# Kernel optimization log

Measured on AMD Instinct MI355X. Metric: run time of the kernel, lower is better.

## Reference

```python
import jax, jax.numpy as jnp
import numpy as np

EPS = 1e-8
LN_EPS = 1e-5
NEG = -1e9
H, E, D, P = 4, 32, 8, 64          # heads, embed_dim, head_dim, particles (= input_dim)
N_LAYERS, N_CLS = 4, 2
N_BATCH = 2048
F_EXTRA = 60                        # x feature channels; F_EXTRA + 4 == P == input_dim


def _ln(x):
    m = jnp.mean(x, -1, keepdims=True)
    v = jnp.mean((x - m) ** 2, -1, keepdims=True)
    return (x - m) * jax.lax.rsqrt(v + LN_EPS)


def _lin(x, w, b):
    return x @ w.T + b


def _gelu(x):
    return jax.nn.gelu(x, approximate=False)


def _mha(q_in, kv, in_w, in_b, out_w, out_b, attn_bias, kpm):
    # torch nn.MultiheadAttention, batch_first=False. q_in: (L,N,E), kv: (S,N,E)
    L, N, _ = q_in.shape
    S = kv.shape[0]
    q = _lin(q_in, in_w[:E], in_b[:E]) * (D ** -0.5)
    k = _lin(kv, in_w[E:2 * E], in_b[E:2 * E])
    v = _lin(kv, in_w[2 * E:], in_b[2 * E:])
    q = q.reshape(L, N, H, D); k = k.reshape(S, N, H, D); v = v.reshape(S, N, H, D)
    s = jnp.einsum('lnhd,snhd->nhls', q, k)
    if attn_bias is not None:
        s = s + attn_bias.reshape(N, H, L, S)
    s = jnp.where(kpm[:, None, None, :], NEG, s)
    a = jax.nn.softmax(s, -1)
    o = jnp.einsum('nhls,snhd->lnhd', a, v).reshape(L, N, E)
    return _lin(o, out_w, out_b)


def _jet_features(v):
    # vectorized calculate_jet_features_; v: (N,4,P). All pair features are symmetric,
    # diagonal stays zero (python loop skipped i==j), features are detached.
    e, px, py, pz = v[:, 0], v[:, 1], v[:, 2], v[:, 3]
    pt = jnp.sqrt(px ** 2 + py ** 2 + EPS)
    y = 0.5 * jnp.log((e + pz + EPS) / (e - pz + EPS))
    phi = jnp.mod(jnp.arctan2(py, px + EPS), 2.0 * np.pi)   # already in [0, 2pi)
    r = lambda a: a[:, :, None]
    c = lambda a: a[:, None, :]
    dist = (r(px) + c(px)) ** 2 + (r(py) + c(py)) ** 2 + (r(pz) + c(pz)) ** 2
    delta = jnp.sqrt(jnp.abs((r(y) - c(y)) ** 2 + (r(phi) - c(phi)) ** 2))
    pmin = jnp.minimum(r(pt), c(pt))
    kt = pmin * delta
    z = pmin / (r(pt) + c(pt) + EPS)
    m2 = r(e) ** 2 + c(e) ** 2 - dist
    f = jnp.stack([delta, kt, z, m2], axis=1)               # (N,4,P,P)
    f = f * (1.0 - jnp.eye(v.shape[2], dtype=f.dtype))
    return jax.lax.stop_gradient(f)


def _conv2d(x, w, b, stride, pad):
    y = jax.lax.conv_general_dilated(x, w, (stride, stride), [(pad, pad), (pad, pad)],
                                     dimension_numbers=('NCHW', 'OIHW', 'NCHW'))
    return y + b[None, :, None, None]


def _forward(x, four_momenta, jet_inputs, bn_w, bn_b, e1_w, e1_b, e2_w, e2_b,
             c1_w, c1_b, c2_w, c2_b,
             pb_in_w, pb_in_b, pb_out_w, pb_out_b, pb_f1_w, pb_f1_b, pb_f2_w, pb_f2_b, pb_wres,
             cb_in_w, cb_in_b, cb_out_w, cb_out_b, cb_f1_w, cb_f1_b, cb_f2_w, cb_f2_b, cb_wres,
             cb_cattn, cls_token, norm_w, norm_b, m1_w, m1_b, mh_w, mh_b, mf_w, mf_b):
    N = x.shape[0]
    xc = jnp.concatenate([x, four_momenta], axis=1)                 # (N, P, P): channels == particles
    kpm = ~(jnp.arange(P)[None, :] < jet_inputs[:, 1][:, None])     # (N, P) True = padded key
    xb = jnp.transpose(xc, (0, 2, 1))                               # (N, C=P, L=input_dim)
    mu = jnp.mean(xb, axis=(0, 2), keepdims=True)
    var = jnp.var(xb, axis=(0, 2), keepdims=True)
    xb = (xb - mu) * jax.lax.rsqrt(var + LN_EPS) * bn_w[None, :, None] + bn_b[None, :, None]
    h = jnp.transpose(xb, (2, 0, 1))                                # (seq, N, P)
    h = _gelu(_lin(_ln(h), e1_w, e1_b))
    h = _gelu(_lin(_ln(h), e2_w, e2_b))                             # (P, N, E)
    # --- PairEmbed: pairwise kinematic features -> 2 convs -> per-head attention bias
    f = _jet_features(four_momenta)                                 # (N, 4, P, P)
    cpe = _conv2d(f, c1_w, c1_b, 4, 0)                              # (N, H, 16, 16)
    cpe = _conv2d(cpe, c2_w, c2_b, 2, 1)                            # (N, H, 9, 9)
    bias = cpe.reshape(N * H, 9, 9)
    bias = jnp.pad(bias, ((0, 0), (0, P - 9), (0, P - 9)))          # additive bias zero-padded to (N*H,P,P)
    # --- particle blocks
    for i in range(N_LAYERS):
        res = h
        a = _ln(h)
        a = _mha(a, a, pb_in_w[i], pb_in_b[i], pb_out_w[i], pb_out_b[i], bias, kpm)
        h = _ln(a) + res
        res = h
        g = _gelu(_lin(_ln(h), pb_f1_w[i], pb_f1_b[i]))
        g = _lin(_ln(g), pb_f2_w[i], pb_f2_b[i])
        h = g + pb_wres[i] * res
    # --- class-attention blocks
    kpm_cls = jnp.concatenate([jnp.zeros((N, 1), dtype=bool), kpm], axis=1)
    cls = jnp.broadcast_to(cls_token, (1, N, E))
    for i in range(N_CLS):
        res = cls
        u = _ln(jnp.concatenate([cls, h], axis=0))                  # pre_attn_norm on keys/values only
        a = _mha(cls, u, cb_in_w[i], cb_in_b[i], cb_out_w[i], cb_out_b[i], None, kpm_cls)
        # tbhd,h->tbdh then reshape flattens as (d, h) order, matching torch
        a = jnp.einsum('tbhd,h->tbdh', a.reshape(1, N, H, D), cb_cattn[i]).reshape(1, N, E)
        cls = _ln(a) + res
        res = cls
        g = _gelu(_lin(_ln(cls), cb_f1_w[i], cb_f1_b[i]))
        g = _lin(_ln(g), cb_f2_w[i], cb_f2_b[i])
        cls = g + cb_wres[i] * res
    # --- head: affine LayerNorm + MLP (the two transposes in MLP cancel)
    z = (_ln(cls) * norm_w + norm_b)[0]                             # (N, E)
    z = jax.nn.relu(_lin(z, m1_w, m1_b))
    z = jax.nn.relu(_lin(z, mh_w, mh_b))
    z = jax.nn.sigmoid(_lin(z, mf_w, mf_b))                         # (N, 1)
    return z.reshape(-1)


def setup_inputs():
    key = jax.random.key(0)
    ks = jax.random.split(key, 40)
    w = lambda k, s: (0.05 * jax.random.normal(k, s)).astype(jnp.float32)
    p3 = jax.random.normal(ks[0], (N_BATCH, 3, P), dtype=jnp.float32)
    en = jnp.sqrt(jnp.sum(p3 ** 2, axis=1, keepdims=True) + 0.1)    # physical: E > |pz|
    four_momenta = jnp.concatenate([en, p3], axis=1)
    return {
        'x': jax.random.normal(ks[1], (N_BATCH, F_EXTRA, P), dtype=jnp.float32),
        'four_momenta': four_momenta,
        'jet_inputs': jax.random.randint(ks[2], (N_BATCH, 2), 1, P + 1),
        'bn_w': jnp.ones((P,), jnp.float32), 'bn_b': jnp.zeros((P,), jnp.float32),
        'e1_w': w(ks[3], (64, P)), 'e1_b': w(ks[4], (64,)),
        'e2_w': w(ks[5], (E, 64)), 'e2_b': w(ks[6], (E,)),
        'c1_w': w(ks[7], (H, 4, 4, 4)), 'c1_b': w(ks[8], (H,)),
        'c2_w': w(ks[9], (H, H, 2, 2)), 'c2_b': w(ks[10], (H,)),
        'pb_in_w': w(ks[11], (N_LAYERS, 3 * E, E)), 'pb_in_b': w(ks[12], (N_LAYERS, 3 * E)),
        'pb_out_w': w(ks[13], (N_LAYERS, E, E)), 'pb_out_b': w(ks[14], (N_LAYERS, E)),
        'pb_f1_w': w(ks[15], (N_LAYERS, 2 * E, E)), 'pb_f1_b': w(ks[16], (N_LAYERS, 2 * E)),
        'pb_f2_w': w(ks[17], (N_LAYERS, E, 2 * E)), 'pb_f2_b': w(ks[18], (N_LAYERS, E)),
        'pb_wres': jnp.ones((N_LAYERS, E), jnp.float32),
        'cb_in_w': w(ks[19], (N_CLS, 3 * E, E)), 'cb_in_b': w(ks[20], (N_CLS, 3 * E)),
        'cb_out_w': w(ks[21], (N_CLS, E, E)), 'cb_out_b': w(ks[22], (N_CLS, E)),
        'cb_f1_w': w(ks[23], (N_CLS, 2 * E, E)), 'cb_f1_b': w(ks[24], (N_CLS, 2 * E)),
        'cb_f2_w': w(ks[25], (N_CLS, E, 2 * E)), 'cb_f2_b': w(ks[26], (N_CLS, E)),
        'cb_wres': jnp.ones((N_CLS, E), jnp.float32),
        'cb_cattn': jnp.ones((N_CLS, H), jnp.float32),
        'cls_token': w(ks[27], (1, 1, E)),
        'norm_w': jnp.ones((E,), jnp.float32), 'norm_b': jnp.zeros((E,), jnp.float32),
        'm1_w': w(ks[28], (32, E)), 'm1_b': w(ks[29], (32,)),
        'mh_w': w(ks[30], (32, 32)), 'mh_b': w(ks[31], (32,)),
        'mf_w': w(ks[32], (1, 32)), 'mf_b': w(ks[33], (1,)),
    }


def reference(x, four_momenta, jet_inputs, bn_w, bn_b, e1_w, e1_b, e2_w, e2_b,
              c1_w, c1_b, c2_w, c2_b,
              pb_in_w, pb_in_b, pb_out_w, pb_out_b, pb_f1_w, pb_f1_b, pb_f2_w, pb_f2_b, pb_wres,
              cb_in_w, cb_in_b, cb_out_w, cb_out_b, cb_f1_w, cb_f1_b, cb_f2_w, cb_f2_b, cb_wres,
              cb_cattn, cls_token, norm_w, norm_b, m1_w, m1_b, mh_w, mh_b, mf_w, mf_b):
    return _forward(x, four_momenta, jet_inputs, bn_w, bn_b, e1_w, e1_b, e2_w, e2_b,
                    c1_w, c1_b, c2_w, c2_b,
                    pb_in_w, pb_in_b, pb_out_w, pb_out_b, pb_f1_w, pb_f1_b, pb_f2_w, pb_f2_b, pb_wres,
                    cb_in_w, cb_in_b, cb_out_w, cb_out_b, cb_f1_w, cb_f1_b, cb_f2_w, cb_f2_b, cb_wres,
                    cb_cattn, cls_token, norm_w, norm_b, m1_w, m1_b, mh_w, mh_b, mf_w, mf_b)
```

## Files before the change

### kernel.cpp

```cpp
#include <hip/hip_runtime.h>


__device__ __forceinline__ float4 ld4(const float* p){ return *reinterpret_cast<const float4*>(p); }
__device__ __forceinline__ void st4(float* p, float4 v){ *reinterpret_cast<float4*>(p) = v; }
__device__ __forceinline__ float dot4(float4 a, float4 b){ return a.x*b.x + a.y*b.y + a.z*b.z + a.w*b.w; }
__device__ __forceinline__ float geluf(float v){ return 0.5f*v*(1.0f + erff(v*0.70710678118654752f)); }

__global__ void bn_stats_partial(const float* __restrict__ x, const float* __restrict__ fm,
                                 float* __restrict__ part) {
  int p  = threadIdx.x & 63;
  int rg = threadIdx.x >> 6;
  float s = 0.f, s2 = 0.f;
  for (int R = blockIdx.x*4 + rg; R < 2048*64; R += 1024) {
    int n_ = R >> 6, c = R & 63;
    float v = (c < 60) ? x[n_*3840 + c*64 + p] : fm[n_*256 + (c-60)*64 + p];
    s += v; s2 += v*v;
  }
  __shared__ float sm[256], sm2[256];
  sm[threadIdx.x] = s; sm2[threadIdx.x] = s2;
  __syncthreads();
  if (threadIdx.x < 64) {
    part[blockIdx.x*128 + p]      = sm[p]+sm[64+p]+sm[128+p]+sm[192+p];
    part[blockIdx.x*128 + 64 + p] = sm2[p]+sm2[64+p]+sm2[128+p]+sm2[192+p];
  }
}

__global__ void bn_stats_final(const float* __restrict__ part, float* __restrict__ stats) {
  int p = threadIdx.x;
  float s = 0.f, s2 = 0.f;
  for (int b = 0; b < 256; b++){ s += part[b*128+p]; s2 += part[b*128+64+p]; }
  float mean = s * (1.f/131072.f);
  float var  = s2 * (1.f/131072.f) - mean*mean;
  stats[p]      = mean;
  stats[64+p]   = rsqrtf(var + 1e-5f);
}

__device__ __forceinline__ void ln_rows32(const float* src, float* dst, int tid){
  int r = tid>>2, g = tid&3;
  const float* row = src + r*36 + g*8;
  float4 a = ld4(row), b = ld4(row+4);
  float s = a.x+a.y+a.z+a.w + b.x+b.y+b.z+b.w;
  s += __shfl_xor(s,1); s += __shfl_xor(s,2);
  float mean = s * 0.03125f;
  float4 da = make_float4(a.x-mean,a.y-mean,a.z-mean,a.w-mean);
  float4 db = make_float4(b.x-mean,b.y-mean,b.z-mean,b.w-mean);
  float q = dot4(da,da) + dot4(db,db);
  q += __shfl_xor(q,1); q += __shfl_xor(q,2);
  float irs = rsqrtf(q*0.03125f + 1e-5f);
  float* drow = dst + r*36 + g*8;
  st4(drow,   make_float4(da.x*irs, da.y*irs, da.z*irs, da.w*irs));
  st4(drow+4, make_float4(db.x*irs, db.y*irs, db.z*irs, db.w*irs));
}

__device__ __forceinline__ void ln_rows64(const float* src, float* dst, int tid){
  int r = tid>>2, g = tid&3;
  const float* row = src + r*68 + g*16;
  float4 v0 = ld4(row), v1 = ld4(row+4), v2 = ld4(row+8), v3 = ld4(row+12);
  float s = v0.x+v0.y+v0.z+v0.w + v1.x+v1.y+v1.z+v1.w
          + v2.x+v2.y+v2.z+v2.w + v3.x+v3.y+v3.z+v3.w;
  s += __shfl_xor(s,1); s += __shfl_xor(s,2);
  float mean = s * 0.015625f;
  float4 d0 = make_float4(v0.x-mean,v0.y-mean,v0.z-mean,v0.w-mean);
  float4 d1 = make_float4(v1.x-mean,v1.y-mean,v1.z-mean,v1.w-mean);
  float4 d2 = make_float4(v2.x-mean,v2.y-mean,v2.z-mean,v2.w-mean);
  float4 d3 = make_float4(v3.x-mean,v3.y-mean,v3.z-mean,v3.w-mean);
  float q = dot4(d0,d0)+dot4(d1,d1)+dot4(d2,d2)+dot4(d3,d3);
  q += __shfl_xor(q,1); q += __shfl_xor(q,2);
  float irs = rsqrtf(q*0.015625f + 1e-5f);
  float* drow = dst + r*68 + g*16;
  st4(drow,    make_float4(d0.x*irs,d0.y*irs,d0.z*irs,d0.w*irs));
  st4(drow+4,  make_float4(d1.x*irs,d1.y*irs,d1.z*irs,d1.w*irs));
  st4(drow+8,  make_float4(d2.x*irs,d2.y*irs,d2.z*irs,d2.w*irs));
  st4(drow+12, make_float4(d3.x*irs,d3.y*irs,d3.z*irs,d3.w*irs));
}

__global__ __launch_bounds__(256) void k_feat(
    const float* __restrict__ fm,
    const float* __restrict__ c1w_g, const float* __restrict__ c1b_g,
    const float* __restrict__ c2w_g, const float* __restrict__ c2b_g,
    float* __restrict__ G_bias)
{
  const int n   = blockIdx.x;
  const int tid = threadIdx.x;
  __shared__ float PQ[448];
  __shared__ float C1O[1024];
  __shared__ float CW[328];

  if (tid < 64) {
    int p = tid;
    float e_  = fm[n*256 + p];
    float px_ = fm[n*256 + 64 + p];
    float py_ = fm[n*256 + 128 + p];
    float pz_ = fm[n*256 + 192 + p];
    float pt_ = sqrtf(px_*px_ + py_*py_ + 1e-8f);
    float y_  = 0.5f * logf((e_ + pz_ + 1e-8f) / (e_ - pz_ + 1e-8f));
    float ph_ = atan2f(py_, px_ + 1e-8f);
    if (ph_ < 0.f) ph_ += 6.283185307179586f;
    PQ[0*64+p]=e_; PQ[1*64+p]=px_; PQ[2*64+p]=py_; PQ[3*64+p]=pz_;
    PQ[4*64+p]=pt_; PQ[5*64+p]=y_; PQ[6*64+p]=ph_;
  }
  CW[tid < 256 ? tid : 0] = c1w_g[tid < 256 ? tid : 0];
  if (tid < 4)  CW[256+tid] = c1b_g[tid];
  if (tid < 64) CW[260+tid] = c2w_g[tid];
  if (tid < 4)  CW[324+tid] = c2b_g[tid];
  __syncthreads();

  {
    int ho = tid>>4, wo = tid&15;
    float a0=0.f,a1=0.f,a2=0.f,a3=0.f;
    #pragma unroll 1
    for (int kh=0; kh<4; kh++){
      int r = ho*4+kh;
      float er=PQ[r], pxr=PQ[64+r], pyr=PQ[128+r], pzr=PQ[192+r], ptr_=PQ[256+r], yr=PQ[320+r], phr=PQ[384+r];
      #pragma unroll
      for (int kw=0; kw<4; kw++){
        int c = wo*4+kw;
        if (r == c) continue;
        float ec=PQ[c], pxc=PQ[64+c], pyc=PQ[128+c], pzc=PQ[192+c], ptc=PQ[256+c], yc=PQ[320+c], phc=PQ[384+c];
        float dy = yr-yc, dp = phr-phc;
        float delta = sqrtf(fabsf(dy*dy + dp*dp));
        float pmin = fminf(ptr_, ptc);
        float kt = pmin * delta;
        float zz = pmin / (ptr_ + ptc + 1e-8f);
        float sx_ = pxr+pxc, sy_ = pyr+pyc, sz_ = pzr+pzc;
        float m2 = er*er + ec*ec - (sx_*sx_ + sy_*sy_ + sz_*sz_);
        int wb = kh*4+kw;
        a0 += delta*CW[0*64+wb] + kt*CW[0*64+16+wb] + zz*CW[0*64+32+wb] + m2*CW[0*64+48+wb];
        a1 += delta*CW[1*64+wb] + kt*CW[1*64+16+wb] + zz*CW[1*64+32+wb] + m2*CW[1*64+48+wb];
        a2 += delta*CW[2*64+wb] + kt*CW[2*64+16+wb] + zz*CW[2*64+32+wb] + m2*CW[2*64+48+wb];
        a3 += delta*CW[3*64+wb] + kt*CW[3*64+16+wb] + zz*CW[3*64+32+wb] + m2*CW[3*64+48+wb];
      }
    }
    C1O[0*256 + tid] = a0 + CW[256+0];
    C1O[1*256 + tid] = a1 + CW[256+1];
    C1O[2*256 + tid] = a2 + CW[256+2];
    C1O[3*256 + tid] = a3 + CW[256+3];
  }
  __syncthreads();

  for (int idx = tid; idx < 324; idx += 256) {
    int co = idx/81, rem = idx%81, i = rem/9, j = rem%9;
    float s = CW[324+co];
    #pragma unroll
    for (int ci=0; ci<4; ci++){
      #pragma unroll
      for (int kh=0; kh<2; kh++){
        int ri = 2*i - 1 + kh;
        if (ri < 0 || ri >= 16) continue;
        #pragma unroll
        for (int kw=0; kw<2; kw++){
          int cj = 2*j - 1 + kw;
          if (cj < 0 || cj >= 16) continue;
          s += CW[260 + co*16 + ci*4 + kh*2 + kw] * C1O[ci*256 + ri*16 + cj];
        }
      }
    }
    G_bias[n*324 + idx] = s;
  }
}

__global__ __launch_bounds__(256, 3) void k_embed2(
    const float* __restrict__ x, const float* __restrict__ fm,
    const float* __restrict__ stats,
    const float* __restrict__ bn_w, const float* __restrict__ bn_b,
    const float* __restrict__ e1w, const float* __restrict__ e1b,
    const float* __restrict__ e2w, const float* __restrict__ e2b,
    float* __restrict__ G_h)
{
  const int n   = blockIdx.x;
  const int tid = threadIdx.x;

  __shared__ __align__(16) float SX[64*68];
  __shared__ __align__(16) float SY[64*68];
  __shared__ __align__(16) float SW[4448];
  __shared__ float SSTAT[128];

  if (tid < 64) {
    float mu = stats[tid], rs = stats[64+tid];
    float sc = rs * bn_w[tid];
    SSTAT[tid]      = sc;
    SSTAT[64+tid]   = bn_b[tid] - mu*sc;
  }
  __syncthreads();

  {
    int p = tid & 63;
    float sc = SSTAT[p], sh = SSTAT[64+p];
    for (int c = tid>>6; c < 64; c += 4) {
      float v = (c < 60) ? x[n*3840 + c*64 + p] : fm[n*256 + (c-60)*64 + p];
      SX[c*68 + p] = v*sc + sh;
    }
  }
  __syncthreads();

  ln_rows64(SX, SY, tid);
  for (int idx = tid; idx < 4096; idx += 256){ SW[(idx>>6)*68 + (idx&63)] = e1w[idx]; }
  for (int idx = tid; idx < 64; idx += 256) SW[4352+idx] = e1b[idx];
  __syncthreads();

  {
    int tg = tid>>4, og = tid&15;
    float acc[4][4];
    #pragma unroll
    for (int o=0;o<4;o++){ float b = SW[4352+o*16+og];
      #pragma unroll
      for (int i=0;i<4;i++) acc[i][o] = b; }
    #pragma unroll 2
    for (int j=0;j<64;j+=4){
      float4 av[4], wv[4];
      #pragma unroll
      for (int i=0;i<4;i++) av[i] = ld4(SY + (tg*4+i)*68 + j);
      #pragma unroll
      for (int o=0;o<4;o++) wv[o] = ld4(SW + (o*16+og)*68 + j);
      #pragma unroll
      for (int i=0;i<4;i++)
        #pragma unroll
        for (int o=0;o<4;o++) acc[i][o] += dot4(av[i], wv[o]);
    }
    __syncthreads();
    #pragma unroll
    for (int i=0;i<4;i++)
      #pragma unroll
      for (int o=0;o<4;o++) SX[(tg*4+i)*68 + o*16+og] = geluf(acc[i][o]);
  }
  __syncthreads();

  ln_rows64(SX, SY, tid);
  for (int idx = tid; idx < 2048; idx += 256){ SW[(idx>>6)*68 + (idx&63)] = e2w[idx]; }
  for (int idx = tid; idx < 32; idx += 256) SW[4352+idx] = e2b[idx];
  __syncthreads();

  {
    int tg = tid>>4, og = tid&15;
    float acc[4][2];
    #pragma unroll
    for (int o=0;o<2;o++){ float b = SW[4352+o*16+og];
      #pragma unroll
      for (int i=0;i<4;i++) acc[i][o] = b; }
    #pragma unroll 2
    for (int j=0;j<64;j+=4){
      float4 av[4], wv[2];
      #pragma unroll
      for (int i=0;i<4;i++) av[i] = ld4(SY + (tg*4+i)*68 + j);
      #pragma unroll
      for (int o=0;o<2;o++) wv[o] = ld4(SW + (o*16+og)*68 + j);
      #pragma unroll
      for (int i=0;i<4;i++)
        #pragma unroll
        for (int o=0;o<2;o++) acc[i][o] += dot4(av[i], wv[o]);
    }
    #pragma unroll
    for (int i=0;i<4;i++)
      #pragma unroll
      for (int o=0;o<2;o++) G_h[n*2048 + (tg*4+i)*32 + o*16+og] = geluf(acc[i][o]);
  }
}

__global__ __launch_bounds__(256, 3) void k_layer(
    const int* __restrict__ ji,
    const float* __restrict__ in_w,  const float* __restrict__ in_b,
    const float* __restrict__ out_w, const float* __restrict__ out_b,
    const float* __restrict__ f1w,   const float* __restrict__ f1b,
    const float* __restrict__ f2w,   const float* __restrict__ f2b,
    const float* __restrict__ wres,
    float* __restrict__ G_h, const float* __restrict__ G_bias)
{
  const int n   = blockIdx.x;
  const int tid = threadIdx.x;

  __shared__ __align__(16) float SH[64*36];
  __shared__ __align__(16) float SX[64*36];
  __shared__ __align__(16) float SY[64*68];
  __shared__ __align__(16) float SW[3584];
  __shared__ float SBIAS[324];
  __shared__ int s_njet;

  if (tid == 0) s_njet = ji[n*2+1];
  for (int idx = tid; idx < 512; idx += 256) {
    float4 v = ld4(G_h + n*2048 + idx*4);
    int t = idx>>3, e = (idx&7)*4;
    st4(&SH[t*36 + e], v);
  }
  for (int idx = tid; idx < 324; idx += 256) SBIAS[idx] = G_bias[n*324 + idx];
  __syncthreads();

  ln_rows32(SH, SX, tid);
  for (int idx = tid; idx < 3072; idx += 256){ SW[(idx>>5)*36 + (idx&31)] = in_w[idx]; }
  for (int idx = tid; idx < 96; idx += 256) SW[3456+idx] = in_b[idx];
  __syncthreads();

  {
    int tg = tid>>4, og = tid&15;
    float acc[4][4];
    #pragma unroll
    for (int o=0;o<4;o++){ float b = SW[3456+32+o*16+og];
      #pragma unroll
      for (int i=0;i<4;i++) acc[i][o] = b; }
    #pragma unroll 2
    for (int j=0;j<32;j+=4){
      float4 av[4], wv[4];
      #pragma unroll
      for (int i=0;i<4;i++) av[i] = ld4(SX + (tg*4+i)*36 + j);
      #pragma unroll
      for (int o=0;o<4;o++) wv[o] = ld4(SW + (32+o*16+og)*36 + j);
      #pragma unroll
      for (int i=0;i<4;i++)
        #pragma unroll
        for (int o=0;o<4;o++) acc[i][o] += dot4(av[i], wv[o]);
    }
    #pragma unroll
    for (int i=0;i<4;i++)
      #pragma unroll
      for (int o=0;o<4;o++){
        int ew = 32 + o*16+og, t = tg*4+i;
        if (ew < 64) SY[(ew-32)*68 + t] = acc[i][o];
        else         SY[2176 + (ew-64)*68 + t] = acc[i][o];
      }
  }
  __syncthreads();

  float od[8];
  {
    int hh = tid>>6, l = tid&63;
    float qd[8];
    #pragma unroll
    for (int d=0;d<8;d++){
      int e = hh*8+d;
      float a_ = SW[3456+e];
      #pragma unroll
      for (int k=0;k<8;k++) a_ += dot4(ld4(SX + l*36 + k*4), ld4(SW + e*36 + k*4));
      qd[d] = a_ * 0.35355339059327373f;
    }
    int njet = s_njet;
    float m = -3.4e38f, lsum = 0.f;
    #pragma unroll
    for (int d=0;d<8;d++) od[d] = 0.f;
    #pragma unroll 1
    for (int s0 = 0; s0 < 64; s0 += 16) {
      float sc[16];
      #pragma unroll
      for (int j=0;j<16;j++) sc[j]=0.f;
      #pragma unroll
      for (int d=0;d<8;d++){
        const float* kr = SY + (hh*8+d)*68 + s0;
        float qv = qd[d];
        #pragma unroll
        for (int j=0;j<16;j+=4){
          float4 kv4 = ld4(kr+j);
          sc[j]  +=qv*kv4.x; sc[j+1]+=qv*kv4.y;
          sc[j+2]+=qv*kv4.z; sc[j+3]+=qv*kv4.w;
        }
      }
      float cm = -3.4e38f;
      #pragma unroll
      for (int j=0;j<16;j++){
        int s = s0+j;
        float a_ = sc[j];
        if (s0 == 0 && l < 9 && j < 9) a_ += SBIAS[hh*81 + l*9 + j];
        a_ = (s >= njet) ? -1000000000.0f : a_;
        sc[j] = a_;
        cm = fmaxf(cm, a_);
      }
      float nm = fmaxf(m, cm);
      float corr = __expf(m - nm);
      lsum *= corr;
      #pragma unroll
      for (int d=0;d<8;d++) od[d] *= corr;
      #pragma unroll
      for (int j=0;j<16;j++){ sc[j] = __expf(sc[j]-nm); lsum += sc[j]; }
      #pragma unroll
      for (int d=0;d<8;d++){
        const float* vr = SY + 2176 + (hh*8+d)*68 + s0;
        float a_ = 0.f;
        #pragma unroll
        for (int j=0;j<16;j+=4){
          float4 vv = ld4(vr+j);
          a_ += sc[j]*vv.x + sc[j+1]*vv.y + sc[j+2]*vv.z + sc[j+3]*vv.w;
        }
        od[d] += a_;
      }
      m = nm;
    }
    float inv = 1.f/lsum;
    #pragma unroll
    for (int d=0;d<8;d++) od[d] *= inv;
  }
  __syncthreads();
  {
    int hh = tid>>6, l = tid&63;
    st4(&SX[l*36 + hh*8],     make_float4(od[0],od[1],od[2],od[3]));
    st4(&SX[l*36 + hh*8 + 4], make_float4(od[4],od[5],od[6],od[7]));
  }
  for (int idx = tid; idx < 1024; idx += 256){ SW[(idx>>5)*36 + (idx&31)] = out_w[idx]; }
  for (int idx = tid; idx < 32; idx += 256) SW[3456+idx] = out_b[idx];
  __syncthreads();

  {
    int tg = tid>>4, og = tid&15;
    float acc[4][2];
    #pragma unroll
    for (int o=0;o<2;o++){ float b = SW[3456+o*16+og];
      #pragma unroll
      for (int i=0;i<4;i++) acc[i][o] = b; }
    #pragma unroll 2
    for (int j=0;j<32;j+=4){
      float4 av[4], wv[2];
      #pragma unroll
      for (int i=0;i<4;i++) av[i] = ld4(SX + (tg*4+i)*36 + j);
      #pragma unroll
      for (int o=0;o<2;o++) wv[o] = ld4(SW + (o*16+og)*36 + j);
      #pragma unroll
      for (int i=0;i<4;i++)
        #pragma unroll
        for (int o=0;o<2;o++) acc[i][o] += dot4(av[i], wv[o]);
    }
    #pragma unroll
    for (int i=0;i<4;i++)
      #pragma unroll
      for (int o=0;o<2;o++) SY[(tg*4+i)*36 + o*16+og] = acc[i][o];
  }
  __syncthreads();

  {
    int r = tid>>2, g = tid&3;
    const float* row = SY + r*36 + g*8;
    float4 a = ld4(row), b = ld4(row+4);
    float s = a.x+a.y+a.z+a.w + b.x+b.y+b.z+b.w;
    s += __shfl_xor(s,1); s += __shfl_xor(s,2);
    float mean = s * 0.03125f;
    float4 da = make_float4(a.x-mean,a.y-mean,a.z-mean,a.w-mean);
    float4 db = make_float4(b.x-mean,b.y-mean,b.z-mean,b.w-mean);
    float q = dot4(da,da) + dot4(db,db);
    q += __shfl_xor(q,1); q += __shfl_xor(q,2);
    float irs = rsqrtf(q*0.03125f + 1e-5f);
    float* hrow = SH + r*36 + g*8;
    float4 ha = ld4(hrow), hb = ld4(hrow+4);
    st4(hrow,   make_float4(da.x*irs+ha.x, da.y*irs+ha.y, da.z*irs+ha.z, da.w*irs+ha.w));
    st4(hrow+4, make_float4(db.x*irs+hb.x, db.y*irs+hb.y, db.z*irs+hb.z, db.w*irs+hb.w));
  }
  __syncthreads();

  ln_rows32(SH, SX, tid);
  for (int idx = tid; idx < 2048; idx += 256){ SW[(idx>>5)*36 + (idx&31)] = f1w[idx]; }
  for (int idx = tid; idx < 64; idx += 256) SW[3456+idx] = f1b[idx];
  __syncthreads();

  {
    int tg = tid>>4, og = tid&15;
    float acc[4][4];
    #pragma unroll
    for (int o=0;o<4;o++){ float b = SW[3456+o*16+og];
      #pragma unroll
      for (int i=0;i<4;i++) acc[i][o] = b; }
    #pragma unroll 2
    for (int j=0;j<32;j+=4){
      float4 av[4], wv[4];
      #pragma unroll
      for (int i=0;i<4;i++) av[i] = ld4(SX + (tg*4+i)*36 + j);
      #pragma unroll
      for (int o=0;o<4;o++) wv[o] = ld4(SW + (o*16+og)*36 + j);
      #pragma unroll
      for (int i=0;i<4;i++)
        #pragma unroll
        for (int o=0;o<4;o++) acc[i][o] += dot4(av[i], wv[o]);
    }
    #pragma unroll
    for (int i=0;i<4;i++)
      #pragma unroll
      for (int o=0;o<4;o++) SY[(tg*4+i)*68 + o*16+og] = geluf(acc[i][o]);
  }
  __syncthreads();

  {
    int r = tid>>2, g = tid&3;
    float* row = SY + r*68 + g*16;
    float4 v0 = ld4(row), v1 = ld4(row+4), v2 = ld4(row+8), v3 = ld4(row+12);
    float s = v0.x+v0.y+v0.z+v0.w + v1.x+v1.y+v1.z+v1.w
            + v2.x+v2.y+v2.z+v2.w + v3.x+v3.y+v3.z+v3.w;
    s += __shfl_xor(s,1); s += __shfl_xor(s,2);
    float mean = s * 0.015625f;
    float4 d0 = make_float4(v0.x-mean,v0.y-mean,v0.z-mean,v0.w-mean);
    float4 d1 = make_float4(v1.x-mean,v1.y-mean,v1.z-mean,v1.w-mean);
    float4 d2 = make_float4(v2.x-mean,v2.y-mean,v2.z-mean,v2.w-mean);
    float4 d3 = make_float4(v3.x-mean,v3.y-mean,v3.z-mean,v3.w-mean);
    float q = dot4(d0,d0)+dot4(d1,d1)+dot4(d2,d2)+dot4(d3,d3);
    q += __shfl_xor(q,1); q += __shfl_xor(q,2);
    float irs = rsqrtf(q*0.015625f + 1e-5f);
    st4(row,    make_float4(d0.x*irs,d0.y*irs,d0.z*irs,d0.w*irs));
    st4(row+4,  make_float4(d1.x*irs,d1.y*irs,d1.z*irs,d1.w*irs));
    st4(row+8,  make_float4(d2.x*irs,d2.y*irs,d2.z*irs,d2.w*irs));
    st4(row+12, make_float4(d3.x*irs,d3.y*irs,d3.z*irs,d3.w*irs));
  }
  for (int idx = tid; idx < 2048; idx += 256){ SW[(idx>>6)*68 + (idx&63)] = f2w[idx]; }
  for (int idx = tid; idx < 32; idx += 256){ SW[3456+idx] = f2b[idx]; SW[3488+idx] = wres[idx]; }
  __syncthreads();

  {
    int tg = tid>>4, og = tid&15;
    float acc[4][2];
    #pragma unroll
    for (int o=0;o<2;o++){ float b = SW[3456+o*16+og];
      #pragma unroll
      for (int i=0;i<4;i++) acc[i][o] = b; }
    #pragma unroll 2
    for (int j=0;j<64;j+=4){
      float4 av[4], wv[2];
      #pragma unroll
      for (int i=0;i<4;i++) av[i] = ld4(SY + (tg*4+i)*68 + j);
      #pragma unroll
      for (int o=0;o<2;o++) wv[o] = ld4(SW + (o*16+og)*68 + j);
      #pragma unroll
      for (int i=0;i<4;i++)
        #pragma unroll
        for (int o=0;o<2;o++) acc[i][o] += dot4(av[i], wv[o]);
    }
    #pragma unroll
    for (int i=0;i<4;i++)
      #pragma unroll
      for (int o=0;o<2;o++){
        int e = o*16+og, t = tg*4+i;
        G_h[n*2048 + t*32 + e] = acc[i][o] + SW[3488+e]*SH[t*36+e];
      }
  }
}

__global__ __launch_bounds__(256, 3) void k_cls(
    const int* __restrict__ ji,
    const float* __restrict__ cb_in_w, const float* __restrict__ cb_in_b,
    const float* __restrict__ cb_out_w, const float* __restrict__ cb_out_b,
    const float* __restrict__ cb_f1_w, const float* __restrict__ cb_f1_b,
    const float* __restrict__ cb_f2_w, const float* __restrict__ cb_f2_b,
    const float* __restrict__ cb_wres, const float* __restrict__ cb_cattn,
    const float* __restrict__ cls_tok, const float* __restrict__ norm_w, const float* __restrict__ norm_b,
    const float* __restrict__ m1w, const float* __restrict__ m1b,
    const float* __restrict__ mhw, const float* __restrict__ mhb,
    const float* __restrict__ mfw, const float* __restrict__ mfb,
    const float* __restrict__ G_h, float* __restrict__ out)
{
  const int n   = blockIdx.x;
  const int tid = threadIdx.x;

  __shared__ __align__(16) float SX[64*36];
  __shared__ __align__(16) float SY[64*68];
  __shared__ __align__(16) float SW[3584];
  __shared__ __align__(16) float SV[320];
  __shared__ __align__(16) float csh[32];
  __shared__ int s_njet;

  if (tid == 0) s_njet = ji[n*2+1];
  for (int idx = tid; idx < 512; idx += 256) {
    float4 v = ld4(G_h + n*2048 + idx*4);
    int t = idx>>3, e = (idx&7)*4;
    st4(&SX[t*36 + e], v);
  }
  __syncthreads();

  ln_rows32(SX, SX, tid);
  if (tid < 32) csh[tid] = cls_tok[tid];
  __syncthreads();

  #pragma unroll 1
  for (int cl = 0; cl < 2; cl++) {
    const float* iw = cb_in_w + cl*3072;
    const float* ib = cb_in_b + cl*96;

    if (tid < 32) {
      float v = csh[tid];
      float s = v;
      s += __shfl_xor(s,1); s += __shfl_xor(s,2); s += __shfl_xor(s,4); s += __shfl_xor(s,8); s += __shfl_xor(s,16);
      float mean = s * 0.03125f;
      float d = v - mean;
      float q = d*d;
      q += __shfl_xor(q,1); q += __shfl_xor(q,2); q += __shfl_xor(q,4); q += __shfl_xor(q,8); q += __shfl_xor(q,16);
      float irs = rsqrtf(q*0.03125f + 1e-5f);
      SV[tid] = d*irs;
    }
    for (int idx = tid; idx < 3072; idx += 256){ SW[(idx>>5)*36 + (idx&31)] = iw[idx]; }
    for (int idx = tid; idx < 96; idx += 256) SW[3456+idx] = ib[idx];
    __syncthreads();

    if (tid < 32) {
      int e = tid;
      float a_ = SW[3456+e];
      #pragma unroll
      for (int k=0;k<8;k++) a_ += dot4(ld4(&csh[k*4]), ld4(SW + e*36 + k*4));
      SV[32+e] = a_ * 0.35355339059327373f;
    }
    if (tid < 64) {
      int ew = 32 + tid;
      float a_ = SW[3456+ew];
      #pragma unroll
      for (int k=0;k<8;k++) a_ += dot4(ld4(SV + k*4), ld4(SW + ew*36 + k*4));
      if (ew < 64) SY[(ew-32)*68] = a_;
      else         SY[2176 + (ew-64)*68] = a_;
    }
    {
      int tg = tid>>4, og = tid&15;
      float acc[4][4];
      #pragma unroll
      for (int o=0;o<4;o++){ float b = SW[3456+32+o*16+og];
        #pragma unroll
        for (int i=0;i<4;i++) acc[i][o] = b; }
      #pragma unroll 2
      for (int j=0;j<32;j+=4){
        float4 av[4], wv[4];
        #pragma unroll
        for (int i=0;i<4;i++) av[i] = ld4(SX + (tg*4+i)*36 + j);
        #pragma unroll
        for (int o=0;o<4;o++) wv[o] = ld4(SW + (32+o*16+og)*36 + j);
        #pragma unroll
        for (int i=0;i<4;i++)
          #pragma unroll
          for (int o=0;o<4;o++) acc[i][o] += dot4(av[i], wv[o]);
      }
      #pragma unroll
      for (int i=0;i<4;i++)
        #pragma unroll
        for (int o=0;o<4;o++){
          int ew = 32 + o*16+og, s = tg*4+i + 1;
          if (ew < 64) SY[(ew-32)*68 + s] = acc[i][o];
          else         SY[2176 + (ew-64)*68 + s] = acc[i][o];
        }
    }
    __syncthreads();

    {
      int hh = tid>>6, l = tid&63;
      int njet = s_njet;
      float q8[8];
      #pragma unroll
      for (int d=0;d<8;d++) q8[d] = SV[32 + hh*8 + d];
      float sc_ = 0.f;
      #pragma unroll
      for (int d=0;d<8;d++) sc_ += q8[d]*SY[(hh*8+d)*68 + l];
      if (l > 0 && (l-1) >= njet) sc_ = -1000000000.0f;
      float sc64 = 0.f;
      if (l == 0){
        #pragma unroll
        for (int d=0;d<8;d++) sc64 += q8[d]*SY[(hh*8+d)*68 + 64];
        if (63 >= njet) sc64 = -1000000000.0f;
      }
      float mx = sc_;
      if (l == 0) mx = fmaxf(mx, sc64);
      mx = fmaxf(mx, __shfl_xor(mx,1));  mx = fmaxf(mx, __shfl_xor(mx,2));
      mx = fmaxf(mx, __shfl_xor(mx,4));  mx = fmaxf(mx, __shfl_xor(mx,8));
      mx = fmaxf(mx, __shfl_xor(mx,16)); mx = fmaxf(mx, __shfl_xor(mx,32));
      float p   = __expf(sc_ - mx);
      float p64 = (l==0) ? __expf(sc64 - mx) : 0.f;
      float ssum = p + p64;
      ssum += __shfl_xor(ssum,1); ssum += __shfl_xor(ssum,2); ssum += __shfl_xor(ssum,4);
      ssum += __shfl_xor(ssum,8); ssum += __shfl_xor(ssum,16); ssum += __shfl_xor(ssum,32);
      float inv = 1.f/ssum;
      #pragma unroll
      for (int d=0;d<8;d++){
        float term = p * SY[2176 + (hh*8+d)*68 + l];
        if (l == 0) term += p64 * SY[2176 + (hh*8+d)*68 + 64];
        term += __shfl_xor(term,1); term += __shfl_xor(term,2); term += __shfl_xor(term,4);
        term += __shfl_xor(term,8); term += __shfl_xor(term,16); term += __shfl_xor(term,32);
        if (l == 0) SV[64 + hh*8 + d] = term*inv;
      }
    }
    __syncthreads();

    if (tid < 32) {
      int e = tid;
      const float* wrow = cb_out_w + (cl*32 + e)*32;
      float a_ = cb_out_b[cl*32 + e];
      #pragma unroll
      for (int j=0;j<32;j++) a_ += SV[64+j]*wrow[j];
      float ca = cb_cattn[cl*4 + (e>>3)];
      SV[96 + (e&7)*4 + (e>>3)] = a_*ca;
    }
    if (tid < 32) {
      float v = SV[96+tid];
      float s = v;
      s += __shfl_xor(s,1); s += __shfl_xor(s,2); s += __shfl_xor(s,4); s += __shfl_xor(s,8); s += __shfl_xor(s,16);
      float mean = s * 0.03125f;
      float d = v - mean;
      float q = d*d;
      q += __shfl_xor(q,1); q += __shfl_xor(q,2); q += __shfl_xor(q,4); q += __shfl_xor(q,8); q += __shfl_xor(q,16);
      float irs = rsqrtf(q*0.03125f + 1e-5f);
      csh[tid] = d*irs + csh[tid];
    }
    if (tid < 32) {
      float v = csh[tid];
      float s = v;
      s += __shfl_xor(s,1); s += __shfl_xor(s,2); s += __shfl_xor(s,4); s += __shfl_xor(s,8); s += __shfl_xor(s,16);
      float mean = s * 0.03125f;
      float d = v - mean;
      float q = d*d;
      q += __shfl_xor(q,1); q += __shfl_xor(q,2); q += __shfl_xor(q,4); q += __shfl_xor(q,8); q += __shfl_xor(q,16);
      float irs = rsqrtf(q*0.03125f + 1e-5f);
      SV[tid] = d*irs;
    }
    if (tid < 64) {
      int o = tid;
      const float* wrow = cb_f1_w + (cl*64+o)*32;
      float a_ = cb_f1_b[cl*64+o];
      #pragma unroll
      for (int j=0;j<32;j++) a_ += SV[j]*wrow[j];
      SV[128+o] = geluf(a_);
    }
    if (tid < 64) {
      float v = SV[128+tid];
      float s = v;
      s += __shfl_xor(s,1); s += __shfl_xor(s,2); s += __shfl_xor(s,4); s += __shfl_xor(s,8);
      s += __shfl_xor(s,16); s += __shfl_xor(s,32);
      float mean = s * 0.015625f;
      float d = v - mean;
      float q = d*d;
      q += __shfl_xor(q,1); q += __shfl_xor(q,2); q += __shfl_xor(q,4); q += __shfl_xor(q,8);
      q += __shfl_xor(q,16); q += __shfl_xor(q,32);
      float irs = rsqrtf(q*0.015625f + 1e-5f);
      SV[192+tid] = d*irs;
    }
    if (tid < 32) {
      int e = tid;
      const float* wrow = cb_f2_w + (cl*32+e)*64;
      float a_ = cb_f2_b[cl*32+e];
      #pragma unroll
      for (int j=0;j<64;j++) a_ += SV[192+j]*wrow[j];
      csh[e] = a_ + cb_wres[cl*32+e]*csh[e];
    }
  }

  if (tid < 32) {
    float v = csh[tid];
    float s = v;
    s += __shfl_xor(s,1); s += __shfl_xor(s,2); s += __shfl_xor(s,4); s += __shfl_xor(s,8); s += __shfl_xor(s,16);
    float mean = s * 0.03125f;
    float d = v - mean;
    float q = d*d;
    q += __shfl_xor(q,1); q += __shfl_xor(q,2); q += __shfl_xor(q,4); q += __shfl_xor(q,8); q += __shfl_xor(q,16);
    float irs = rsqrtf(q*0.03125f + 1e-5f);
    SV[tid] = d*irs*norm_w[tid] + norm_b[tid];
  }
  if (tid < 32) {
    float a_ = m1b[tid];
    const float* wrow = m1w + tid*32;
    #pragma unroll
    for (int j=0;j<32;j++) a_ += SV[j]*wrow[j];
    SV[64+tid] = fmaxf(a_, 0.f);
  }
  if (tid < 32) {
    float a_ = mhb[tid];
    const float* wrow = mhw + tid*32;
    #pragma unroll
    for (int j=0;j<32;j++) a_ += SV[64+j]*wrow[j];
    SV[128+tid] = fmaxf(a_, 0.f);
  }
  if (tid == 0) {
    float a_ = mfb[0];
    #pragma unroll
    for (int j=0;j<32;j++) a_ += SV[128+j]*mfw[j];
    out[n] = 1.f/(1.f + expf(-a_));
  }
}

extern "C" void kernel_launch(void* const* d_in, const int* in_sizes, int n_in,
                              void* d_out, int out_size, void* d_ws, size_t ws_size,
                              hipStream_t stream) {
  (void)in_sizes; (void)n_in; (void)out_size; (void)ws_size;
  const float* x     = (const float*)d_in[0];
  const float* fm    = (const float*)d_in[1];
  const int*   ji    = (const int*)  d_in[2];
  const float* bn_w  = (const float*)d_in[3];
  const float* bn_b  = (const float*)d_in[4];
  const float* e1w   = (const float*)d_in[5];
  const float* e1b   = (const float*)d_in[6];
  const float* e2w   = (const float*)d_in[7];
  const float* e2b   = (const float*)d_in[8];
  const float* c1w   = (const float*)d_in[9];
  const float* c1b   = (const float*)d_in[10];
  const float* c2w   = (const float*)d_in[11];
  const float* c2b   = (const float*)d_in[12];
  const float* pb_in_w  = (const float*)d_in[13];
  const float* pb_in_b  = (const float*)d_in[14];
  const float* pb_out_w = (const float*)d_in[15];
  const float* pb_out_b = (const float*)d_in[16];
  const float* pb_f1_w  = (const float*)d_in[17];
  const float* pb_f1_b  = (const float*)d_in[18];
  const float* pb_f2_w  = (const float*)d_in[19];
  const float* pb_f2_b  = (const float*)d_in[20];
  const float* pb_wres  = (const float*)d_in[21];
  const float* cb_in_w  = (const float*)d_in[22];
  const float* cb_in_b  = (const float*)d_in[23];
  const float* cb_out_w = (const float*)d_in[24];
  const float* cb_out_b = (const float*)d_in[25];
  const float* cb_f1_w  = (const float*)d_in[26];
  const float* cb_f1_b  = (const float*)d_in[27];
  const float* cb_f2_w  = (const float*)d_in[28];
  const float* cb_f2_b  = (const float*)d_in[29];
  const float* cb_wres  = (const float*)d_in[30];
  const float* cb_cattn = (const float*)d_in[31];
  const float* cls_tok  = (const float*)d_in[32];
  const float* norm_w   = (const float*)d_in[33];
  const float* norm_b   = (const float*)d_in[34];
  const float* m1w      = (const float*)d_in[35];
  const float* m1b      = (const float*)d_in[36];
  const float* mhw      = (const float*)d_in[37];
  const float* mhb      = (const float*)d_in[38];
  const float* mfw      = (const float*)d_in[39];
  const float* mfb      = (const float*)d_in[40];

  float* part   = (float*)d_ws;
  float* stats  = part + 32768;
  float* G_h    = part + 40960;
  float* G_bias = G_h + 2048*2048;

  bn_stats_partial<<<256, 256, 0, stream>>>(x, fm, part);
  bn_stats_final<<<1, 64, 0, stream>>>(part, stats);
  k_feat<<<2048, 256, 0, stream>>>(fm, c1w, c1b, c2w, c2b, G_bias);
  k_embed2<<<2048, 256, 0, stream>>>(x, fm, stats, bn_w, bn_b, e1w, e1b, e2w, e2b, G_h);
  for (int li = 0; li < 4; li++) {
    k_layer<<<2048, 256, 0, stream>>>(ji,
        pb_in_w + li*3072, pb_in_b + li*96,
        pb_out_w + li*1024, pb_out_b + li*32,
        pb_f1_w + li*2048, pb_f1_b + li*64,
        pb_f2_w + li*2048, pb_f2_b + li*32,
        pb_wres + li*32, G_h, G_bias);
  }
  k_cls<<<2048, 256, 0, stream>>>(ji, cb_in_w, cb_in_b, cb_out_w, cb_out_b,
                                  cb_f1_w, cb_f1_b, cb_f2_w, cb_f2_b,
                                  cb_wres, cb_cattn, cls_tok, norm_w, norm_b,
                                  m1w, m1b, mhw, mhb, mfw, mfb, G_h, (float*)d_out);
}
```

Measured before the change: 540.8 us.

## Fuse jet feature conv kernel into embed kernel and vectorize weight staging

Merges k_feat into the embedding kernel, aliasing its scratch buffers onto SY so one launch computes both the pair-feature conv bias and the embedding MLP. Weight and bias staging into shared memory is switched from scalar to float4 loads in every kernel, the input BN load is vectorized, and one redundant barrier is removed. In k_layer the attention bias moves from a shared-memory table into per-thread registers (b9). This saves a launch and some load instructions, at the cost of more registers and shared-memory pressure in the fused kernel.

After: 537.5 us. No clear change (-0.6%).

```diff
diff --git a/kernel.cpp b/kernel.cpp
--- a/kernel.cpp
+++ b/kernel.cpp
@@ -74,18 +74,34 @@
   st4(drow+12, make_float4(d3.x*irs,d3.y*irs,d3.z*irs,d3.w*irs));
 }
 
-__global__ __launch_bounds__(256) void k_feat(
-    const float* __restrict__ fm,
+__global__ __launch_bounds__(256, 3) void k_embed(
+    const float* __restrict__ x, const float* __restrict__ fm,
+    const float* __restrict__ stats,
+    const float* __restrict__ bn_w, const float* __restrict__ bn_b,
+    const float* __restrict__ e1w, const float* __restrict__ e1b,
+    const float* __restrict__ e2w, const float* __restrict__ e2b,
     const float* __restrict__ c1w_g, const float* __restrict__ c1b_g,
     const float* __restrict__ c2w_g, const float* __restrict__ c2b_g,
-    float* __restrict__ G_bias)
+    float* __restrict__ G_h, float* __restrict__ G_bias)
 {
   const int n   = blockIdx.x;
   const int tid = threadIdx.x;
-  __shared__ float PQ[448];
-  __shared__ float C1O[1024];
-  __shared__ float CW[328];
-
+
+  __shared__ __align__(16) float SX[64*68];
+  __shared__ __align__(16) float SY[64*68];
+  __shared__ __align__(16) float SW[4448];
+  __shared__ float SSTAT[128];
+
+  float* PQ  = SY;
+  float* C1O = SY + 448;
+  float* CW  = SY + 1472;
+
+  if (tid < 64) {
+    float mu = stats[tid], rs = stats[64+tid];
+    float sc = rs * bn_w[tid];
+    SSTAT[tid]      = sc;
+    SSTAT[64+tid]   = bn_b[tid] - mu*sc;
+  }
   if (tid < 64) {
     int p = tid;
     float e_  = fm[n*256 + p];
@@ -99,7 +115,7 @@
     PQ[0*64+p]=e_; PQ[1*64+p]=px_; PQ[2*64+p]=py_; PQ[3*64+p]=pz_;
     PQ[4*64+p]=pt_; PQ[5*64+p]=y_; PQ[6*64+p]=ph_;
   }
-  CW[tid < 256 ? tid : 0] = c1w_g[tid < 256 ? tid : 0];
+  CW[tid] = c1w_g[tid];
   if (tid < 4)  CW[256+tid] = c1b_g[tid];
   if (tid < 64) CW[260+tid] = c2w_g[tid];
   if (tid < 4)  CW[324+tid] = c2b_g[tid];
@@ -157,45 +173,20 @@
     }
     G_bias[n*324 + idx] = s;
   }
-}
-
-__global__ __launch_bounds__(256, 3) void k_embed2(
-    const float* __restrict__ x, const float* __restrict__ fm,
-    const float* __restrict__ stats,
-    const float* __restrict__ bn_w, const float* __restrict__ bn_b,
-    const float* __restrict__ e1w, const float* __restrict__ e1b,
-    const float* __restrict__ e2w, const float* __restrict__ e2b,
-    float* __restrict__ G_h)
-{
-  const int n   = blockIdx.x;
-  const int tid = threadIdx.x;
-
-  __shared__ __align__(16) float SX[64*68];
-  __shared__ __align__(16) float SY[64*68];
-  __shared__ __align__(16) float SW[4448];
-  __shared__ float SSTAT[128];
-
-  if (tid < 64) {
-    float mu = stats[tid], rs = stats[64+tid];
-    float sc = rs * bn_w[tid];
-    SSTAT[tid]      = sc;
-    SSTAT[64+tid]   = bn_b[tid] - mu*sc;
-  }
-  __syncthreads();
-
-  {
-    int p = tid & 63;
-    float sc = SSTAT[p], sh = SSTAT[64+p];
-    for (int c = tid>>6; c < 64; c += 4) {
-      float v = (c < 60) ? x[n*3840 + c*64 + p] : fm[n*256 + (c-60)*64 + p];
-      SX[c*68 + p] = v*sc + sh;
+  {
+    int p4 = (tid & 15) * 4;
+    float sc0 = SSTAT[p4], sc1 = SSTAT[p4+1], sc2 = SSTAT[p4+2], sc3 = SSTAT[p4+3];
+    float sh0 = SSTAT[64+p4], sh1 = SSTAT[64+p4+1], sh2 = SSTAT[64+p4+2], sh3 = SSTAT[64+p4+3];
+    for (int c = tid>>4; c < 64; c += 16) {
+      float4 v = (c < 60) ? ld4(x + n*3840 + c*64 + p4) : ld4(fm + n*256 + (c-60)*64 + p4);
+      st4(&SX[c*68 + p4], make_float4(v.x*sc0+sh0, v.y*sc1+sh1, v.z*sc2+sh2, v.w*sc3+sh3));
     }
   }
   __syncthreads();
 
   ln_rows64(SX, SY, tid);
-  for (int idx = tid; idx < 4096; idx += 256){ SW[(idx>>6)*68 + (idx&63)] = e1w[idx]; }
-  for (int idx = tid; idx < 64; idx += 256) SW[4352+idx] = e1b[idx];
+  for (int idx = tid; idx < 1024; idx += 256) st4(&SW[(idx>>4)*68 + (idx&15)*4], ld4(e1w + idx*4));
+  if (tid < 64) SW[4352+tid] = e1b[tid];
   __syncthreads();
 
   {
@@ -217,7 +208,6 @@
         #pragma unroll
         for (int o=0;o<4;o++) acc[i][o] += dot4(av[i], wv[o]);
     }
-    __syncthreads();
     #pragma unroll
     for (int i=0;i<4;i++)
       #pragma unroll
@@ -226,8 +216,8 @@
   __syncthreads();
 
   ln_rows64(SX, SY, tid);
-  for (int idx = tid; idx < 2048; idx += 256){ SW[(idx>>6)*68 + (idx&63)] = e2w[idx]; }
-  for (int idx = tid; idx < 32; idx += 256) SW[4352+idx] = e2b[idx];
+  for (int idx = tid; idx < 512; idx += 256) st4(&SW[(idx>>4)*68 + (idx&15)*4], ld4(e2w + idx*4));
+  if (tid < 32) SW[4352+tid] = e2b[tid];
   __syncthreads();
 
   {
@@ -272,21 +262,30 @@
   __shared__ __align__(16) float SX[64*36];
   __shared__ __align__(16) float SY[64*68];
   __shared__ __align__(16) float SW[3584];
-  __shared__ float SBIAS[324];
   __shared__ int s_njet;
 
   if (tid == 0) s_njet = ji[n*2+1];
+  float b9[9];
+  {
+    int hh = tid>>6, l = tid&63;
+    if (l < 9) {
+      #pragma unroll
+      for (int j=0;j<9;j++) b9[j] = G_bias[n*324 + hh*81 + l*9 + j];
+    } else {
+      #pragma unroll
+      for (int j=0;j<9;j++) b9[j] = 0.f;
+    }
+  }
   for (int idx = tid; idx < 512; idx += 256) {
     float4 v = ld4(G_h + n*2048 + idx*4);
     int t = idx>>3, e = (idx&7)*4;
     st4(&SH[t*36 + e], v);
   }
-  for (int idx = tid; idx < 324; idx += 256) SBIAS[idx] = G_bias[n*324 + idx];
   __syncthreads();
 
   ln_rows32(SH, SX, tid);
-  for (int idx = tid; idx < 3072; idx += 256){ SW[(idx>>5)*36 + (idx&31)] = in_w[idx]; }
-  for (int idx = tid; idx < 96; idx += 256) SW[3456+idx] = in_b[idx];
+  for (int idx = tid; idx < 768; idx += 256) st4(&SW[(idx>>3)*36 + (idx&7)*4], ld4(in_w + idx*4));
+  if (tid < 96) SW[3456+tid] = in_b[tid];
   __syncthreads();
 
   {
@@ -356,7 +355,7 @@
       for (int j=0;j<16;j++){
         int s = s0+j;
         float a_ = sc[j];
-        if (s0 == 0 && l < 9 && j < 9) a_ += SBIAS[hh*81 + l*9 + j];
+        if (s0 == 0 && l < 9 && j < 9) a_ += b9[j];
         a_ = (s >= njet) ? -1000000000.0f : a_;
         sc[j] = a_;
         cm = fmaxf(cm, a_);
@@ -391,8 +390,8 @@
     st4(&SX[l*36 + hh*8],     make_float4(od[0],od[1],od[2],od[3]));
     st4(&SX[l*36 + hh*8 + 4], make_float4(od[4],od[5],od[6],od[7]));
   }
-  for (int idx = tid; idx < 1024; idx += 256){ SW[(idx>>5)*36 + (idx&31)] = out_w[idx]; }
-  for (int idx = tid; idx < 32; idx += 256) SW[3456+idx] = out_b[idx];
+  for (int idx = tid; idx < 256; idx += 256) st4(&SW[(idx>>3)*36 + (idx&7)*4], ld4(out_w + idx*4));
+  if (tid < 32) SW[3456+tid] = out_b[tid];
   __syncthreads();
 
   {
@@ -441,8 +440,8 @@
   __syncthreads();
 
   ln_rows32(SH, SX, tid);
-  for (int idx = tid; idx < 2048; idx += 256){ SW[(idx>>5)*36 + (idx&31)] = f1w[idx]; }
-  for (int idx = tid; idx < 64; idx += 256) SW[3456+idx] = f1b[idx];
+  for (int idx = tid; idx < 512; idx += 256) st4(&SW[(idx>>3)*36 + (idx&7)*4], ld4(f1w + idx*4));
+  if (tid < 64) SW[3456+tid] = f1b[tid];
   __syncthreads();
 
   {
@@ -491,8 +490,8 @@
     st4(row+8,  make_float4(d2.x*irs,d2.y*irs,d2.z*irs,d2.w*irs));
     st4(row+12, make_float4(d3.x*irs,d3.y*irs,d3.z*irs,d3.w*irs));
   }
-  for (int idx = tid; idx < 2048; idx += 256){ SW[(idx>>6)*68 + (idx&63)] = f2w[idx]; }
-  for (int idx = tid; idx < 32; idx += 256){ SW[3456+idx] = f2b[idx]; SW[3488+idx] = wres[idx]; }
+  for (int idx = tid; idx < 512; idx += 256) st4(&SW[(idx>>4)*68 + (idx&15)*4], ld4(f2w + idx*4));
+  if (tid < 32){ SW[3456+tid] = f2b[tid]; SW[3488+tid] = wres[tid]; }
   __syncthreads();
 
   {
@@ -575,8 +574,8 @@
       float irs = rsqrtf(q*0.03125f + 1e-5f);
       SV[tid] = d*irs;
     }
-    for (int idx = tid; idx < 3072; idx += 256){ SW[(idx>>5)*36 + (idx&31)] = iw[idx]; }
-    for (int idx = tid; idx < 96; idx += 256) SW[3456+idx] = ib[idx];
+    for (int idx = tid; idx < 768; idx += 256) st4(&SW[(idx>>3)*36 + (idx&7)*4], ld4(iw + idx*4));
+    if (tid < 96) SW[3456+tid] = ib[tid];
     __syncthreads();
 
     if (tid < 32) {
@@ -810,8 +809,8 @@
 
   bn_stats_partial<<<256, 256, 0, stream>>>(x, fm, part);
   bn_stats_final<<<1, 64, 0, stream>>>(part, stats);
-  k_feat<<<2048, 256, 0, stream>>>(fm, c1w, c1b, c2w, c2b, G_bias);
-  k_embed2<<<2048, 256, 0, stream>>>(x, fm, stats, bn_w, bn_b, e1w, e1b, e2w, e2b, G_h);
+  k_embed<<<2048, 256, 0, stream>>>(x, fm, stats, bn_w, bn_b, e1w, e1b, e2w, e2b,
+                                    c1w, c1b, c2w, c2b, G_h, G_bias);
   for (int li = 0; li < 4; li++) {
     k_layer<<<2048, 256, 0, stream>>>(ji,
         pb_in_w + li*3072, pb_in_b + li*96,
```
